# Kernel tuning notes

Hardware: AMD Instinct MI355X
Metric: run time of the kernel (lower is better)

## Reference

```python
import jax, jax.numpy as jnp
import numpy as np

B, HQ, HKV, D, T = 32, 32, 8, 128, 2048
POOL = B * T
SCALING = 0.08838834764831845  # 1/sqrt(128)
LOGIT_CAP = 30.0
NEG = -1e30


def setup_inputs() -> dict:
    key = jax.random.key(0)
    ks = jax.random.split(key, 6)
    q = jax.random.normal(ks[0], (B, HQ * D), dtype=jnp.float32)
    k = jax.random.normal(ks[1], (B, HKV * D), dtype=jnp.float32)
    v = jax.random.normal(ks[2], (B, HKV * D), dtype=jnp.float32)
    k_buffer = jax.random.normal(ks[3], (POOL, HKV, D), dtype=jnp.float32)
    v_buffer = jax.random.normal(ks[4], (POOL, HKV, D), dtype=jnp.float32)
    # each request r owns contiguous pool slots [r*T, (r+1)*T)
    req_to_token = jnp.arange(POOL, dtype=jnp.int64).reshape(B, T)
    req_pool_indices = jnp.arange(B, dtype=jnp.int64)
    seq_lens = jax.random.randint(ks[5], (B,), 1, T + 1, dtype=jnp.int64)
    # the newly decoded token's KV slot is the last in-context slot
    out_cache_loc = req_pool_indices * T + seq_lens - 1
    return {
        "q": q, "k": k, "v": v,
        "k_buffer": k_buffer, "v_buffer": v_buffer,
        "req_to_token": req_to_token,
        "req_pool_indices": req_pool_indices,
        "seq_lens": seq_lens,
        "out_cache_loc": out_cache_loc,
    }


def reference(q, k, v, k_buffer, v_buffer, req_to_token, req_pool_indices,
              seq_lens, out_cache_loc):
    # store_kv_cache: scatter new token KV into the paged pool
    kb = k_buffer.at[out_cache_loc].set(k.reshape(B, HKV, D))
    vb = v_buffer.at[out_cache_loc].set(v.reshape(B, HKV, D))
    # gather each request's paged KV: idx [B, T]
    idx = req_to_token[req_pool_indices]
    K = kb[idx]  # [B, T, HKV, D]
    V = vb[idx]  # [B, T, HKV, D]
    # GQA: group HQ//HKV query heads per kv head
    qh = q.reshape(B, HKV, HQ // HKV, D)
    s = jnp.einsum('bkgd,btkd->bkgt', qh, K) * SCALING
    # logit soft cap (logit_cap > 0 branch)
    s = LOGIT_CAP * jnp.tanh(s / LOGIT_CAP)
    mask = jnp.arange(T)[None, :] < seq_lens[:, None]  # [B, T]
    s = jnp.where(mask[:, None, None, :], s, NEG)
    p = jax.nn.softmax(s, axis=-1)
    o = jnp.einsum('bkgt,btkd->bkgd', p, V)
    return o.reshape(B, HQ * D)
```

## Files before the change

### kernel.cpp

```cpp
#include <hip/hip_runtime.h>
#include <hip/hip_bf16.h>

#define NB 32
#define NHQ 32
#define NHKV 8
#define GQ 4
#define DD 128
#define TT 2048
#define NSPLIT 8
#define CHUNK 256

__device__ __forceinline__ float warp_max(float v) {
#pragma unroll
    for (int o = 32; o >= 1; o >>= 1) v = fmaxf(v, __shfl_xor(v, o));
    return v;
}
__device__ __forceinline__ float warp_sum(float v) {
#pragma unroll
    for (int o = 32; o >= 1; o >>= 1) v += __shfl_xor(v, o);
    return v;
}

__global__ __launch_bounds__(256) void attn_part_kernel(
    const float* __restrict__ q,
    const float* __restrict__ knew,
    const float* __restrict__ vnew,
    const float* __restrict__ kbuf,
    const float* __restrict__ vbuf,
    const int* __restrict__ req_to_token,
    const int* __restrict__ req_pool_indices,
    const int* __restrict__ seq_lens,
    const int* __restrict__ out_cache_loc,
    float* __restrict__ part_o,
    float* __restrict__ part_ml)
{
    const int tid   = threadIdx.x;
    const int split = blockIdx.x;
    const int kv    = blockIdx.y;
    const int b     = blockIdx.z;

    const int sl = seq_lens[b];
    const int t0 = split * CHUNK;
    const int nt = min(sl - t0, CHUNK);

    float* po  = part_o  + (((size_t)b * NHKV + kv) * GQ) * NSPLIT * DD;
    float* pml = part_ml + (((size_t)b * NHKV + kv) * GQ) * NSPLIT * 2;

    if (nt <= 0) {
        for (int i = tid; i < GQ * DD; i += 256) {
            const int g = i >> 7, d = i & 127;
            po[(g * NSPLIT + split) * DD + d] = 0.f;
        }
        if (tid < GQ) {
            pml[(tid * NSPLIT + split) * 2 + 0] = -1e30f;
            pml[(tid * NSPLIT + split) * 2 + 1] = 0.f;
        }
        return;
    }

    __shared__ __align__(16) float qs[GQ][DD];
    __shared__ float ps[GQ][CHUNK];
    __shared__ int   slot_s[CHUNK];
    __shared__ float redm[GQ][4];
    __shared__ float msh[GQ], lsh[GQ];
    __shared__ __align__(16) float opart[4][GQ][DD];

    const float* qb = q + ((size_t)b * NHQ + kv * GQ) * DD;
    for (int i = tid; i < GQ * DD; i += 256) qs[i >> 7][i & 127] = qb[i];

    const int req = req_pool_indices[b];
    const int ocl = out_cache_loc[b];
    __syncthreads();

    constexpr float SCALING   = 0.08838834764831845f;
    constexpr float LOGIT_CAP = 30.0f;
    float sc0, sc1, sc2, sc3;
    {
        const int t = tid;
        if (t < nt) {
            const int slot = req_to_token[(size_t)req * TT + t0 + t];
            slot_s[t] = slot;
            const float* krow = (slot == ocl)
                ? (knew + ((size_t)b * NHKV + kv) * DD)
                : (kbuf + ((size_t)slot * NHKV + kv) * DD);
            float d0 = 0.f, d1 = 0.f, d2 = 0.f, d3 = 0.f;
#pragma unroll 8
            for (int d = 0; d < DD; d += 4) {
                const float4 kk = *(const float4*)(krow + d);
                const float4 q0 = *(const float4*)(&qs[0][d]);
                const float4 q1 = *(const float4*)(&qs[1][d]);
                const float4 q2 = *(const float4*)(&qs[2][d]);
                const float4 q3 = *(const float4*)(&qs[3][d]);
                d0 += kk.x * q0.x + kk.y * q0.y + kk.z * q0.z + kk.w * q0.w;
                d1 += kk.x * q1.x + kk.y * q1.y + kk.z * q1.z + kk.w * q1.w;
                d2 += kk.x * q2.x + kk.y * q2.y + kk.z * q2.z + kk.w * q2.w;
                d3 += kk.x * q3.x + kk.y * q3.y + kk.z * q3.z + kk.w * q3.w;
            }
            const float c = SCALING / LOGIT_CAP;
            sc0 = LOGIT_CAP * tanhf(d0 * c);
            sc1 = LOGIT_CAP * tanhf(d1 * c);
            sc2 = LOGIT_CAP * tanhf(d2 * c);
            sc3 = LOGIT_CAP * tanhf(d3 * c);
        } else {
            sc0 = sc1 = sc2 = sc3 = -1e30f;
        }
    }

    float scs[GQ] = {sc0, sc1, sc2, sc3};
#pragma unroll
    for (int g = 0; g < GQ; g++) {
        const float m = warp_max(scs[g]);
        if ((tid & 63) == 0) redm[g][tid >> 6] = m;
    }
    __syncthreads();
    if (tid < GQ) {
        const float* r = redm[tid];
        msh[tid] = fmaxf(fmaxf(r[0], r[1]), fmaxf(r[2], r[3]));
    }
    __syncthreads();
#pragma unroll
    for (int g = 0; g < GQ; g++) {
        const float p = (tid < nt) ? __expf(scs[g] - msh[g]) : 0.f;
        ps[g][tid] = p;
        const float l = warp_sum(p);
        if ((tid & 63) == 0) redm[g][tid >> 6] = l;
    }
    __syncthreads();
    if (tid < GQ) {
        const float* r = redm[tid];
        lsh[tid] = r[0] + r[1] + r[2] + r[3];
    }
    __syncthreads();

    {
        const int w = tid >> 6, lane = tid & 63;
        const int d0 = lane << 1;
        float a0x = 0.f, a0y = 0.f, a1x = 0.f, a1y = 0.f;
        float a2x = 0.f, a2y = 0.f, a3x = 0.f, a3y = 0.f;
        const float* vnewrow = vnew + ((size_t)b * NHKV + kv) * DD;
        for (int t = w; t < nt; t += 4) {
            const int slot = slot_s[t];
            const float* vrow = (slot == ocl)
                ? vnewrow
                : (vbuf + ((size_t)slot * NHKV + kv) * DD);
            const float2 vv = *(const float2*)(vrow + d0);
            const float p0 = ps[0][t], p1 = ps[1][t], p2 = ps[2][t], p3 = ps[3][t];
            a0x += p0 * vv.x; a0y += p0 * vv.y;
            a1x += p1 * vv.x; a1y += p1 * vv.y;
            a2x += p2 * vv.x; a2y += p2 * vv.y;
            a3x += p3 * vv.x; a3y += p3 * vv.y;
        }
        *(float2*)&opart[w][0][d0] = make_float2(a0x, a0y);
        *(float2*)&opart[w][1][d0] = make_float2(a1x, a1y);
        *(float2*)&opart[w][2][d0] = make_float2(a2x, a2y);
        *(float2*)&opart[w][3][d0] = make_float2(a3x, a3y);
    }
    __syncthreads();
    for (int i = tid; i < GQ * DD; i += 256) {
        const int g = i >> 7, d = i & 127;
        const float s = opart[0][g][d] + opart[1][g][d] + opart[2][g][d] + opart[3][g][d];
        po[(g * NSPLIT + split) * DD + d] = s;
    }
    if (tid < GQ) {
        pml[(tid * NSPLIT + split) * 2 + 0] = msh[tid];
        pml[(tid * NSPLIT + split) * 2 + 1] = lsh[tid];
    }
}

__global__ __launch_bounds__(128) void attn_combine_kernel(
    const float* __restrict__ part_o,
    const float* __restrict__ part_ml,
    float* __restrict__ out)
{
    const int h  = blockIdx.x;
    const int d  = threadIdx.x;
    const int b  = h >> 5;
    const int hq = h & 31;

    const float* ml = part_ml + ((size_t)b * NHKV * GQ + hq) * NSPLIT * 2;
    float M = -1e30f;
#pragma unroll
    for (int s = 0; s < NSPLIT; s++) M = fmaxf(M, ml[s * 2]);
    float L = 0.f;
#pragma unroll
    for (int s = 0; s < NSPLIT; s++) L += ml[s * 2 + 1] * __expf(ml[s * 2] - M);

    const float* po = part_o + ((size_t)b * NHKV * GQ + hq) * NSPLIT * DD;
    float acc = 0.f;
#pragma unroll
    for (int s = 0; s < NSPLIT; s++) acc += po[s * DD + d] * __expf(ml[s * 2] - M);

    out[((size_t)b * NHQ + hq) * DD + d] = acc / L;
}

extern "C" void kernel_launch(void* const* d_in, const int* in_sizes, int n_in,
                              void* d_out, int out_size, void* d_ws, size_t ws_size,
                              hipStream_t stream) {
    (void)in_sizes; (void)n_in; (void)out_size; (void)ws_size;
    const float* q    = (const float*)d_in[0];
    const float* k    = (const float*)d_in[1];
    const float* v    = (const float*)d_in[2];
    const float* kbuf = (const float*)d_in[3];
    const float* vbuf = (const float*)d_in[4];
    const int* req_to_token     = (const int*)d_in[5];
    const int* req_pool_indices = (const int*)d_in[6];
    const int* seq_lens         = (const int*)d_in[7];
    const int* out_cache_loc    = (const int*)d_in[8];
    float* out = (float*)d_out;

    float* part_o  = (float*)d_ws;
    float* part_ml = part_o + (size_t)NB * NHKV * GQ * NSPLIT * DD;

    dim3 g1(NSPLIT, NHKV, NB), b1(256);
    attn_part_kernel<<<g1, b1, 0, stream>>>(q, k, v, kbuf, vbuf,
        req_to_token, req_pool_indices, seq_lens, out_cache_loc,
        part_o, part_ml);

    dim3 g2(NB * NHQ), b2(128);
    attn_combine_kernel<<<g2, b2, 0, stream>>>(part_o, part_ml, out);
}
```

Baseline: 525.7 us.

## Coalesce K and V loads by splitting rows across lanes, use fast tanh

QK scoring now has four lanes share each K row, each reading strided float4 segments, then reduces the partial dots with shuffles. This replaces the old one-thread-per-row pattern, whose loads are poorly coalesced. The PV loop uses float4 V loads with two tokens per wave and a cross-half shuffle reduction. Slot indices are prefetched into shared memory, tanhf is replaced with an exp-based approximation, and the score buffer is padded. The exp-based tanh can lose accuracy and overflow for large inputs, though the soft cap keeps inputs bounded. Slot indices are read for all 256 positions even past the sequence length, but these stay inside the request's row.

```diff
diff --git a/kernel.cpp b/kernel.cpp
--- a/kernel.cpp
+++ b/kernel.cpp
@@ -9,6 +9,7 @@
 #define TT 2048
 #define NSPLIT 8
 #define CHUNK 256
+#define PSLD 260
 
 __device__ __forceinline__ float warp_max(float v) {
 #pragma unroll
@@ -19,6 +20,10 @@
 #pragma unroll
     for (int o = 32; o >= 1; o >>= 1) v += __shfl_xor(v, o);
     return v;
+}
+__device__ __forceinline__ float fast_tanh(float x) {
+    const float e = __expf(2.0f * x);
+    return 1.0f - 2.0f / (e + 1.0f);
 }
 
 __global__ __launch_bounds__(256) void attn_part_kernel(
@@ -59,7 +64,7 @@
     }
 
     __shared__ __align__(16) float qs[GQ][DD];
-    __shared__ float ps[GQ][CHUNK];
+    __shared__ float ps[GQ][PSLD];
     __shared__ int   slot_s[CHUNK];
     __shared__ float redm[GQ][4];
     __shared__ float msh[GQ], lsh[GQ];
@@ -67,50 +72,58 @@
 
     const float* qb = q + ((size_t)b * NHQ + kv * GQ) * DD;
     for (int i = tid; i < GQ * DD; i += 256) qs[i >> 7][i & 127] = qb[i];
-
     const int req = req_pool_indices[b];
     const int ocl = out_cache_loc[b];
-    __syncthreads();
+    slot_s[tid] = req_to_token[(size_t)req * TT + t0 + tid];
+    __syncthreads();
+
+    const int lane = tid & 63, w = tid >> 6;
+    const float* knewrow = knew + ((size_t)b * NHKV + kv) * DD;
+    const float* vnewrow = vnew + ((size_t)b * NHKV + kv) * DD;
 
     constexpr float SCALING   = 0.08838834764831845f;
     constexpr float LOGIT_CAP = 30.0f;
-    float sc0, sc1, sc2, sc3;
-    {
-        const int t = tid;
-        if (t < nt) {
-            const int slot = req_to_token[(size_t)req * TT + t0 + t];
-            slot_s[t] = slot;
-            const float* krow = (slot == ocl)
-                ? (knew + ((size_t)b * NHKV + kv) * DD)
-                : (kbuf + ((size_t)slot * NHKV + kv) * DD);
-            float d0 = 0.f, d1 = 0.f, d2 = 0.f, d3 = 0.f;
-#pragma unroll 8
-            for (int d = 0; d < DD; d += 4) {
-                const float4 kk = *(const float4*)(krow + d);
-                const float4 q0 = *(const float4*)(&qs[0][d]);
-                const float4 q1 = *(const float4*)(&qs[1][d]);
-                const float4 q2 = *(const float4*)(&qs[2][d]);
-                const float4 q3 = *(const float4*)(&qs[3][d]);
-                d0 += kk.x * q0.x + kk.y * q0.y + kk.z * q0.z + kk.w * q0.w;
-                d1 += kk.x * q1.x + kk.y * q1.y + kk.z * q1.z + kk.w * q1.w;
-                d2 += kk.x * q2.x + kk.y * q2.y + kk.z * q2.z + kk.w * q2.w;
-                d3 += kk.x * q3.x + kk.y * q3.y + kk.z * q3.z + kk.w * q3.w;
-            }
-            const float c = SCALING / LOGIT_CAP;
-            sc0 = LOGIT_CAP * tanhf(d0 * c);
-            sc1 = LOGIT_CAP * tanhf(d1 * c);
-            sc2 = LOGIT_CAP * tanhf(d2 * c);
-            sc3 = LOGIT_CAP * tanhf(d3 * c);
-        } else {
-            sc0 = sc1 = sc2 = sc3 = -1e30f;
-        }
-    }
-
-    float scs[GQ] = {sc0, sc1, sc2, sc3};
-#pragma unroll
-    for (int g = 0; g < GQ; g++) {
-        const float m = warp_max(scs[g]);
-        if ((tid & 63) == 0) redm[g][tid >> 6] = m;
+    const float cmul = SCALING / LOGIT_CAP;
+
+    const int a = lane & 3;
+    float wm0 = -1e30f, wm1 = -1e30f, wm2 = -1e30f, wm3 = -1e30f;
+    for (int p = 0; p < 4; ++p) {
+        const int tg   = (w << 6) + (p << 4) + (lane >> 2);
+        const int slot = slot_s[tg];
+        const float* krow = (slot == ocl)
+            ? knewrow : (kbuf + ((size_t)slot * NHKV + kv) * DD);
+        float d0 = 0.f, d1 = 0.f, d2 = 0.f, d3 = 0.f;
+#pragma unroll
+        for (int kk = 0; kk < 8; ++kk) {
+            const int off = kk * 16 + a * 4;
+            const float4 kk4 = *(const float4*)(krow + off);
+            const float4 q0 = *(const float4*)(&qs[0][off]);
+            const float4 q1 = *(const float4*)(&qs[1][off]);
+            const float4 q2 = *(const float4*)(&qs[2][off]);
+            const float4 q3 = *(const float4*)(&qs[3][off]);
+            d0 += kk4.x * q0.x + kk4.y * q0.y + kk4.z * q0.z + kk4.w * q0.w;
+            d1 += kk4.x * q1.x + kk4.y * q1.y + kk4.z * q1.z + kk4.w * q1.w;
+            d2 += kk4.x * q2.x + kk4.y * q2.y + kk4.z * q2.z + kk4.w * q2.w;
+            d3 += kk4.x * q3.x + kk4.y * q3.y + kk4.z * q3.z + kk4.w * q3.w;
+        }
+        d0 += __shfl_xor(d0, 1); d0 += __shfl_xor(d0, 2);
+        d1 += __shfl_xor(d1, 1); d1 += __shfl_xor(d1, 2);
+        d2 += __shfl_xor(d2, 1); d2 += __shfl_xor(d2, 2);
+        d3 += __shfl_xor(d3, 1); d3 += __shfl_xor(d3, 2);
+        float s0 = LOGIT_CAP * fast_tanh(d0 * cmul);
+        float s1 = LOGIT_CAP * fast_tanh(d1 * cmul);
+        float s2 = LOGIT_CAP * fast_tanh(d2 * cmul);
+        float s3 = LOGIT_CAP * fast_tanh(d3 * cmul);
+        if (tg >= nt) { s0 = s1 = s2 = s3 = -1e30f; }
+        wm0 = fmaxf(wm0, s0); wm1 = fmaxf(wm1, s1);
+        wm2 = fmaxf(wm2, s2); wm3 = fmaxf(wm3, s3);
+        const float sa = (a == 0) ? s0 : (a == 1) ? s1 : (a == 2) ? s2 : s3;
+        ps[a][tg] = sa;
+    }
+    wm0 = warp_max(wm0); wm1 = warp_max(wm1);
+    wm2 = warp_max(wm2); wm3 = warp_max(wm3);
+    if (lane == 0) {
+        redm[0][w] = wm0; redm[1][w] = wm1; redm[2][w] = wm2; redm[3][w] = wm3;
     }
     __syncthreads();
     if (tid < GQ) {
@@ -118,42 +131,55 @@
         msh[tid] = fmaxf(fmaxf(r[0], r[1]), fmaxf(r[2], r[3]));
     }
     __syncthreads();
-#pragma unroll
-    for (int g = 0; g < GQ; g++) {
-        const float p = (tid < nt) ? __expf(scs[g] - msh[g]) : 0.f;
-        ps[g][tid] = p;
-        const float l = warp_sum(p);
-        if ((tid & 63) == 0) redm[g][tid >> 6] = l;
+
+    {
+        const float m0 = msh[0], m1 = msh[1], m2 = msh[2], m3 = msh[3];
+        const bool valid = tid < nt;
+        float p0 = valid ? __expf(ps[0][tid] - m0) : 0.f;
+        float p1 = valid ? __expf(ps[1][tid] - m1) : 0.f;
+        float p2 = valid ? __expf(ps[2][tid] - m2) : 0.f;
+        float p3 = valid ? __expf(ps[3][tid] - m3) : 0.f;
+        ps[0][tid] = p0; ps[1][tid] = p1; ps[2][tid] = p2; ps[3][tid] = p3;
+        p0 = warp_sum(p0); p1 = warp_sum(p1); p2 = warp_sum(p2); p3 = warp_sum(p3);
+        if (lane == 0) {
+            redm[0][w] = p0; redm[1][w] = p1; redm[2][w] = p2; redm[3][w] = p3;
+        }
     }
     __syncthreads();
     if (tid < GQ) {
         const float* r = redm[tid];
         lsh[tid] = r[0] + r[1] + r[2] + r[3];
     }
-    __syncthreads();
 
     {
-        const int w = tid >> 6, lane = tid & 63;
-        const int d0 = lane << 1;
-        float a0x = 0.f, a0y = 0.f, a1x = 0.f, a1y = 0.f;
-        float a2x = 0.f, a2y = 0.f, a3x = 0.f, a3y = 0.f;
-        const float* vnewrow = vnew + ((size_t)b * NHKV + kv) * DD;
-        for (int t = w; t < nt; t += 4) {
+        const int hs = tid >> 5;
+        const int dl = (tid & 31) << 2;
+        float4 a0 = {0,0,0,0}, a1 = {0,0,0,0}, a2 = {0,0,0,0}, a3 = {0,0,0,0};
+        for (int t = hs; t < nt; t += 8) {
             const int slot = slot_s[t];
             const float* vrow = (slot == ocl)
-                ? vnewrow
-                : (vbuf + ((size_t)slot * NHKV + kv) * DD);
-            const float2 vv = *(const float2*)(vrow + d0);
+                ? vnewrow : (vbuf + ((size_t)slot * NHKV + kv) * DD);
+            const float4 vv = *(const float4*)(vrow + dl);
             const float p0 = ps[0][t], p1 = ps[1][t], p2 = ps[2][t], p3 = ps[3][t];
-            a0x += p0 * vv.x; a0y += p0 * vv.y;
-            a1x += p1 * vv.x; a1y += p1 * vv.y;
-            a2x += p2 * vv.x; a2y += p2 * vv.y;
-            a3x += p3 * vv.x; a3y += p3 * vv.y;
-        }
-        *(float2*)&opart[w][0][d0] = make_float2(a0x, a0y);
-        *(float2*)&opart[w][1][d0] = make_float2(a1x, a1y);
-        *(float2*)&opart[w][2][d0] = make_float2(a2x, a2y);
-        *(float2*)&opart[w][3][d0] = make_float2(a3x, a3y);
+            a0.x += p0 * vv.x; a0.y += p0 * vv.y; a0.z += p0 * vv.z; a0.w += p0 * vv.w;
+            a1.x += p1 * vv.x; a1.y += p1 * vv.y; a1.z += p1 * vv.z; a1.w += p1 * vv.w;
+            a2.x += p2 * vv.x; a2.y += p2 * vv.y; a2.z += p2 * vv.z; a2.w += p2 * vv.w;
+            a3.x += p3 * vv.x; a3.y += p3 * vv.y; a3.z += p3 * vv.z; a3.w += p3 * vv.w;
+        }
+        a0.x += __shfl_xor(a0.x, 32); a0.y += __shfl_xor(a0.y, 32);
+        a0.z += __shfl_xor(a0.z, 32); a0.w += __shfl_xor(a0.w, 32);
+        a1.x += __shfl_xor(a1.x, 32); a1.y += __shfl_xor(a1.y, 32);
+        a1.z += __shfl_xor(a1.z, 32); a1.w += __shfl_xor(a1.w, 32);
+        a2.x += __shfl_xor(a2.x, 32); a2.y += __shfl_xor(a2.y, 32);
+        a2.z += __shfl_xor(a2.z, 32); a2.w += __shfl_xor(a2.w, 32);
+        a3.x += __shfl_xor(a3.x, 32); a3.y += __shfl_xor(a3.y, 32);
+        a3.z += __shfl_xor(a3.z, 32); a3.w += __shfl_xor(a3.w, 32);
+        if ((tid & 32) == 0) {
+            *(float4*)&opart[w][0][dl] = a0;
+            *(float4*)&opart[w][1][dl] = a1;
+            *(float4*)&opart[w][2][dl] = a2;
+            *(float4*)&opart[w][3][dl] = a3;
+        }
     }
     __syncthreads();
     for (int i = tid; i < GQ * DD; i += 256) {
```

After: 543.5 us. +3.4%, slower.
